# Kernel optimization log

Hardware: AMD Instinct MI355X
Metric: run time of the kernel (lower is better)

## Reference

```python
import jax, jax.numpy as jnp
import numpy as np

SQRT2 = 1.4142135623730951
T, B, C, H, W = 4, 8, 256, 32, 32
NB, D = 16, 16  # FL_blocks, block_size = dim // FL_blocks
VTH = 0.5       # all l1/l2 spike thresholds default to 0.5
TAUS = (0.01, 0.02, 0.02, 0.05)  # l2 channel-sparsity taus for LL,HL,LH,HH

# Heaviside spike with ATan surrogate gradient (spikingjelly default, alpha=2)
@jax.custom_vjp
def spike(x):
    return (x >= 0.0).astype(x.dtype)

def _spike_fwd(x):
    return spike(x), x

def _spike_bwd(x, g):
    alpha = 2.0
    sg = (alpha / 2.0) / (1.0 + (jnp.pi / 2.0 * alpha * x) ** 2)
    return (g * sg,)

spike.defvjp(_spike_fwd, _spike_bwd)

def lif(x, tau=2.0):
    # MultiStepLIFNode: v += (x - v)/tau, fire at vth=1, hard reset, detach_reset
    def step(v, xt):
        v = v + (xt - v) / tau
        s = spike(v - 1.0)
        v = v * (1.0 - jax.lax.stop_gradient(s))
        return v, s
    _, s = jax.lax.scan(step, jnp.zeros_like(x[0]), x)
    return s

def bn(x, g, b, eps=1e-5):
    # BatchNorm2d in training mode (batch statistics), x: (N,C,H,W)
    m = x.mean((0, 2, 3), keepdims=True)
    v = x.var((0, 2, 3), keepdims=True)
    return (x - m) / jnp.sqrt(v + eps) * g[None, :, None, None] + b[None, :, None, None]

def conv2d(x, w, b):
    y = jax.lax.conv_general_dilated(x, w, (1, 1), 'SAME',
                                     dimension_numbers=('NCHW', 'OIHW', 'NCHW'))
    return y + b[None, :, None, None]

def coeff_gate(c, vth):
    # spike-thresholded wavelet coefficient: keep coeff where |coeff| >= vth
    return c * spike(jnp.abs(c) - vth)

def channel_gate(c, tau):
    # 'channel' sparsity mode: drop whole channels whose mean energy < tau
    e = jnp.mean(c * c, axis=(0, 1, 3, 4))
    return c * spike(e - tau)[None, None, :, None, None]

def fwd(x, haar_weight, conv1_w, conv1_b, conv2_w, conv2_b,
        g_fwd, b_fwd, g_mul, b_mul, g_inv, b_inv, g_c1, b_c1, g_c2, b_c2):
    Tn, Bn, Cn, Hn, Wn = x.shape
    H2, W2 = Hn // 2, Wn // 2
    TB = Tn * Bn
    xs = lif(x)
    # level-1 Haar along W, spike-gated low/high subbands -> (T,B,2C,H,W/2)
    lo = (xs[..., 0::2] + xs[..., 1::2]) / SQRT2
    hi = (xs[..., 0::2] - xs[..., 1::2]) / SQRT2
    h1 = jnp.concatenate([coeff_gate(lo, VTH), coeff_gate(hi, VTH)], axis=2)
    h1 = bn(h1.reshape(TB, 2 * Cn, Hn, W2), g_fwd, b_fwd).reshape(Tn, Bn, 2 * Cn, Hn, W2)
    # level-2 Haar along H -> LL,HL,LH,HH each (T,B,C,H/2,W/2)
    L, Hc = h1[:, :, :Cn], h1[:, :, Cn:]
    def hh(t):
        return ((t[:, :, :, 0::2] + t[:, :, :, 1::2]) / SQRT2,
                (t[:, :, :, 0::2] - t[:, :, :, 1::2]) / SQRT2)
    LL, HL = hh(L)
    LH, HH = hh(Hc)
    subs = [channel_gate(coeff_gate(c, VTH), tau)
            for c, tau in zip((LL, HL, LH, HH), TAUS)]
    h2 = jnp.concatenate(subs, axis=2)  # (T,B,4C,H/2,W/2)
    h2 = bn(h2.reshape(TB, 4 * Cn, H2, W2), g_mul, b_mul).reshape(Tn, Bn, 4 * Cn, H2, W2)
    # block-diagonal mixing: exactly the torch reshape/permute/einsum path
    haar = h2.reshape(TB, NB, 4 * D, H2, W2).transpose(0, 3, 4, 1, 2)  # (TB,H2,W2,NB,4D)
    parts = [jnp.einsum('thwbd,bdk->thwbk', haar[..., i * D:(i + 1) * D], haar_weight)
             for i in range(4)]
    haar = jnp.concatenate(parts, axis=-1)
    haar = haar.reshape(TB, H2, W2, 4 * Cn).transpose(0, 3, 1, 2).reshape(Tn, Bn, 4 * Cn, H2, W2)
    # inverse 2-level Haar -> (T,B,C,H,W)
    LLr, HLr, LHr, HHr = (haar[:, :, i * Cn:(i + 1) * Cn] for i in range(4))
    def inv_h(a, b):
        e = (a + b) / SQRT2
        o = (a - b) / SQRT2
        return jnp.stack([e, o], axis=-2).reshape(Tn, Bn, Cn, Hn, W2)
    Lr = inv_h(LLr, HLr)
    Hr = inv_h(LHr, HHr)
    e = (Lr + Hr) / SQRT2
    o = (Lr - Hr) / SQRT2
    rec = jnp.stack([e, o], axis=-1).reshape(Tn, Bn, Cn, Hn, Wn)
    rec = bn(rec.reshape(TB, Cn, Hn, Wn), g_inv, b_inv).reshape(Tn, Bn, Cn, Hn, Wn)
    # per-block conv residual branches on the spike tensor
    xr = xs.reshape(TB * NB, D, Hn, Wn)
    c1 = bn(conv2d(xr, conv1_w, conv1_b).reshape(TB, Cn, Hn, Wn), g_c1, b_c1).reshape(Tn, Bn, Cn, Hn, Wn)
    c2 = bn(conv2d(xr, conv2_w, conv2_b).reshape(TB, Cn, Hn, Wn), g_c2, b_c2).reshape(Tn, Bn, Cn, Hn, Wn)
    return rec + c1 + c2

def setup_inputs() -> dict:
    key = jax.random.key(0)
    ks = jax.random.split(key, 4)
    return {
        'x': jax.random.normal(ks[0], (T, B, C, H, W), jnp.float32),
        'haar_weight': 0.02 * jax.random.normal(ks[1], (NB, D, D), jnp.float32),
        'conv1_w': 0.1 * jax.random.normal(ks[2], (D, D, 1, 1), jnp.float32),
        'conv1_b': jnp.zeros((D,), jnp.float32),
        'conv2_w': 0.05 * jax.random.normal(ks[3], (D, D, 3, 3), jnp.float32),
        'conv2_b': jnp.zeros((D,), jnp.float32),
        'g_fwd': jnp.ones((2 * C,), jnp.float32), 'b_fwd': jnp.zeros((2 * C,), jnp.float32),
        'g_mul': jnp.ones((4 * C,), jnp.float32), 'b_mul': jnp.zeros((4 * C,), jnp.float32),
        'g_inv': jnp.ones((C,), jnp.float32), 'b_inv': jnp.zeros((C,), jnp.float32),
        'g_c1': jnp.ones((C,), jnp.float32), 'b_c1': jnp.zeros((C,), jnp.float32),
        'g_c2': jnp.ones((C,), jnp.float32), 'b_c2': jnp.zeros((C,), jnp.float32),
    }

def reference(x, haar_weight, conv1_w, conv1_b, conv2_w, conv2_b,
              g_fwd, b_fwd, g_mul, b_mul, g_inv, b_inv, g_c1, b_c1, g_c2, b_c2):
    return fwd(x, haar_weight, conv1_w, conv1_b, conv2_w, conv2_b,
               g_fwd, b_fwd, g_mul, b_mul, g_inv, b_inv, g_c1, b_c1, g_c2, b_c2)
```

## Files before the change

kernel.cpp:

```cpp
#include <hip/hip_runtime.h>

#define T_ 4
#define B_ 8
#define C_ 256
#define TB_ 32
#define SQRT2_ 1.4142135623730951
#define INVS2_ 0.7071067811865475
#define EPS_ 1e-5

typedef __attribute__((ext_vector_type(8))) short short8;
typedef __attribute__((ext_vector_type(4))) float f32x4;

#define XST_OFF  ((size_t)0)
#define H1C_OFF  ((size_t)16777216)
#define COEF_OFF ((size_t)25165824)
#define ST_OFF   ((size_t)41943040)
#define WTAB_OFF ((size_t)42532864)
#define HIST_OFF ((size_t)42555392)
#define S3S 3072
#define S3Q 3328
#define S4S 3584
#define S4Q 3840
#define S5S 4096
#define S5Q 4352
#define NST 4608
#define NREP 16
#define NHREP 32

__device__ __forceinline__ unsigned short f2bf(float v) {
    union { float f; unsigned u; } x; x.f = v;
    unsigned r = x.u + 0x7FFFu + ((x.u >> 16) & 1u);
    return (unsigned short)(r >> 16);
}

__device__ __forceinline__ double st_sum(const double* __restrict__ st, int idx) {
    double s = 0.0;
    #pragma unroll
    for (int r = 0; r < NREP; ++r) s += st[r * NST + idx];
    return s;
}

__device__ __forceinline__ void mix_frags_q(const float* __restrict__ hw, int gbq, int lane, short8 am[4]) {
    const int o = lane & 15, g = lane >> 4;
    #pragma unroll
    for (int q = 0; q < 4; ++q) {
        #pragma unroll
        for (int e = 0; e < 8; ++e) {
            const int kk = g * 8 + e;
            unsigned short v = 0;
            if ((kk >> 4) == (q & 1)) {
                const int d = kk & 15;
                const int nbp = q * 4 + gbq;
                v = f2bf(hw[(nbp * 16 + d) * 16 + o]);
            }
            am[q][e] = (short)v;
        }
    }
}

__device__ __forceinline__ void conv_frags(const float* __restrict__ w1, const float* __restrict__ w2w,
                                           int lane, short8* awc2, short8& awc1) {
    const int o = lane & 15, g = lane >> 4, dA = (g & 1) * 8;
    #pragma unroll
    for (int m = 0; m < 5; ++m) {
        const int t = (m < 4) ? (2 * m + (g >> 1)) : 8;
        const bool act = (m < 4) || (g < 2);
        #pragma unroll
        for (int j = 0; j < 8; ++j) {
            const float wv = act ? w2w[(o * 16 + dA + j) * 9 + t] : 0.0f;
            awc2[m][j] = (short)f2bf(wv);
        }
    }
    #pragma unroll
    for (int j = 0; j < 8; ++j) {
        const float wv = (g < 2) ? w1[o * 16 + dA + j] : 0.0f;
        awc1[j] = (short)f2bf(wv);
    }
}

__device__ __forceinline__ void load_conv_frags(const unsigned short* __restrict__ convW,
                                                int lane, short8* awc2, short8& awc1) {
    #pragma unroll
    for (int m = 0; m < 5; ++m) awc2[m] = *(const short8*)&convW[(m * 64 + lane) * 8];
    awc1 = *(const short8*)&convW[(5 * 64 + lane) * 8];
}
__device__ __forceinline__ void load_mix_frags(const unsigned short* __restrict__ mixW,
                                               int gbq, int lane, short8 am[4]) {
    #pragma unroll
    for (int q = 0; q < 4; ++q) am[q] = *(const short8*)&mixW[((gbq * 4 + q) * 64 + lane) * 8];
}

__global__ __launch_bounds__(256) void k1_lif(const float* __restrict__ x,
                                              unsigned short* __restrict__ xsT,
                                              signed char* __restrict__ h1c,
                                              int* __restrict__ hist,
                                              double* __restrict__ st,
                                              const float* __restrict__ w1, const float* __restrict__ w2w,
                                              const float* __restrict__ hw,
                                              unsigned short* __restrict__ convW,
                                              unsigned short* __restrict__ mixW) {
    const int q = blockIdx.x & 3, nb = (blockIdx.x >> 2) & 15, b = blockIdx.x >> 6;
    const int tid = threadIdx.x;
    if (tid < 72) {
        double2 z2; z2.x = 0.0; z2.y = 0.0;
        *(double2*)(st + (size_t)blockIdx.x * 144 + tid * 2) = z2;
    }
    const int d = tid >> 4, pg = tid & 15;
    const int c = nb * 16 + d;
    const int h = q * 8 + (pg >> 1), wseg = (pg & 1) * 16;
    __shared__ __align__(16) char tr[8192];
    double v[16];
    #pragma unroll
    for (int i = 0; i < 16; ++i) v[i] = 0.0;
    unsigned long long cs = 0, cdd = 0, cu = 0, cv = 0;
    for (int t = 0; t < T_; ++t) {
        const size_t xi = ((size_t)((t * 8 + b) * 256 + c)) * 1024 + h * 32 + wseg;
        const float4* xp = (const float4*)(x + xi);
        int sp[16];
        #pragma unroll
        for (int q4 = 0; q4 < 4; ++q4) {
            const float4 xv = xp[q4];
            #pragma unroll
            for (int e = 0; e < 4; ++e) {
                const double xd = (e == 0 ? xv.x : e == 1 ? xv.y : e == 2 ? xv.z : xv.w);
                double vv = v[q4 * 4 + e];
                vv = vv + (xd - vv) * 0.5;
                const int s = (vv - 1.0 >= 0.0) ? 1 : 0;
                if (s) vv = 0.0;
                v[q4 * 4 + e] = vv;
                sp[q4 * 4 + e] = s;
            }
        }
        unsigned lo8[2] = {0u, 0u}, hi8[2] = {0u, 0u}, hp8[2] = {0u, 0u};
        #pragma unroll
        for (int pr = 0; pr < 8; ++pr) {
            const int lo = sp[2 * pr] + sp[2 * pr + 1];
            const int hi = sp[2 * pr] - sp[2 * pr + 1];
            const int sh = 8 * (pr & 3);
            lo8[pr >> 2] |= (unsigned)(lo & 0xFF) << sh;
            hi8[pr >> 2] |= (unsigned)(hi & 0xFF) << sh;
            hp8[pr >> 2] |= (unsigned)(hi + 1) << sh;
        }
        const size_t lob = ((size_t)((t * 8 + b) * 512 + c)) * 512 + h * 16 + (pg & 1) * 8;
        const size_t hib = ((size_t)((t * 8 + b) * 512 + 256 + c)) * 512 + h * 16 + (pg & 1) * 8;
        *(uint2*)(h1c + lob) = make_uint2(lo8[0], lo8[1]);
        *(uint2*)(h1c + hib) = make_uint2(hi8[0], hi8[1]);
        const unsigned plo0 = __shfl_xor(lo8[0], 2, 64);
        const unsigned plo1 = __shfl_xor(lo8[1], 2, 64);
        const unsigned php0 = __shfl_xor(hp8[0], 2, 64);
        const unsigned php1 = __shfl_xor(hp8[1], 2, 64);
        if (!(pg & 2)) {
            const unsigned sw0 = lo8[0] + plo0, sw1 = lo8[1] + plo1;
            const unsigned dw0 = lo8[0] + (0x02020202u - plo0), dw1 = lo8[1] + (0x02020202u - plo1);
            const unsigned uw0 = hp8[0] + php0, uw1 = hp8[1] + php1;
            const unsigned vw0 = hp8[0] + (0x02020202u - php0), vw1 = hp8[1] + (0x02020202u - php1);
            #pragma unroll
            for (int j = 0; j < 4; ++j) {
                const int sh = 8 * j;
                cs  += 1ull << (12 * ((sw0 >> sh) & 0x7));
                cs  += 1ull << (12 * ((sw1 >> sh) & 0x7));
                cdd += 1ull << (12 * ((dw0 >> sh) & 0x7));
                cdd += 1ull << (12 * ((dw1 >> sh) & 0x7));
                cu  += 1ull << (12 * ((uw0 >> sh) & 0x7));
                cu  += 1ull << (12 * ((uw1 >> sh) & 0x7));
                cv  += 1ull << (12 * ((vw0 >> sh) & 0x7));
                cv  += 1ull << (12 * ((vw1 >> sh) & 0x7));
            }
        }
        unsigned u[8];
        #pragma unroll
        for (int k = 0; k < 8; ++k)
            u[k] = (sp[2 * k] ? 0x3F80u : 0u) | (sp[2 * k + 1] ? 0x3F800000u : 0u);
        const int base = d * 512 + pg * 32;
        const int sw = (d & 3) << 4;
        *(uint4*)(tr + ((base) ^ sw))      = make_uint4(u[0], u[1], u[2], u[3]);
        *(uint4*)(tr + ((base + 16) ^ sw)) = make_uint4(u[4], u[5], u[6], u[7]);
        __syncthreads();
        {
            const int p = tid;
            unsigned o[8];
            #pragma unroll
            for (int dd = 0; dd < 8; ++dd) {
                const unsigned short a0 = *(const unsigned short*)(tr + (2 * dd) * 512 + (((p << 1)) ^ (((2 * dd) & 3) << 4)));
                const unsigned short a1 = *(const unsigned short*)(tr + (2 * dd + 1) * 512 + (((p << 1)) ^ (((2 * dd + 1) & 3) << 4)));
                o[dd] = (unsigned)a0 | ((unsigned)a1 << 16);
            }
            unsigned short* dst = xsT + (((size_t)((t * 8 + b) * 16 + nb)) * 1024 + q * 256 + p) * 16;
            *(uint4*)dst = make_uint4(o[0], o[1], o[2], o[3]);
            *(uint4*)(dst + 8) = make_uint4(o[4], o[5], o[6], o[7]);
        }
        __syncthreads();
    }
    #pragma unroll
    for (int m = 1; m < 16; m <<= 1) {
        {
            const unsigned a = __shfl_xor((unsigned)cs, m, 64);
            const unsigned bb2 = __shfl_xor((unsigned)(cs >> 32), m, 64);
            cs += ((unsigned long long)bb2 << 32) | a;
        }
        {
            const unsigned a = __shfl_xor((unsigned)cdd, m, 64);
            const unsigned bb2 = __shfl_xor((unsigned)(cdd >> 32), m, 64);
            cdd += ((unsigned long long)bb2 << 32) | a;
        }
        {
            const unsigned a = __shfl_xor((unsigned)cu, m, 64);
            const unsigned bb2 = __shfl_xor((unsigned)(cu >> 32), m, 64);
            cu += ((unsigned long long)bb2 << 32) | a;
        }
        {
            const unsigned a = __shfl_xor((unsigned)cv, m, 64);
            const unsigned bb2 = __shfl_xor((unsigned)(cv >> 32), m, 64);
            cv += ((unsigned long long)bb2 << 32) | a;
        }
    }
    if (pg == 0) {
        int* hh = hist + ((size_t)(b * 4 + q) * 20) * 256 + c;
        #pragma unroll
        for (int k = 0; k < 5; ++k) {
            hh[k * 256]         = (int)((cs  >> (12 * k)) & 0xFFF);
            hh[(5 + k) * 256]   = (int)((cdd >> (12 * k)) & 0xFFF);
            hh[(10 + k) * 256]  = (int)((cu  >> (12 * k)) & 0xFFF);
            hh[(15 + k) * 256]  = (int)((cv  >> (12 * k)) & 0xFFF);
        }
    }
    if (blockIdx.x == 0) {
        const int lane = tid & 63, grp = tid >> 6;
        if (grp == 0) {
            short8 awc2[5], awc1;
            conv_frags(w1, w2w, lane, awc2, awc1);
            #pragma unroll
            for (int m = 0; m < 5; ++m) *(short8*)&convW[(m * 64 + lane) * 8] = awc2[m];
            *(short8*)&convW[(5 * 64 + lane) * 8] = awc1;
        }
        short8 am[4];
        mix_frags_q(hw, grp, lane, am);
        #pragma unroll
        for (int qq = 0; qq < 4; ++qq) *(short8*)&mixW[((grp * 4 + qq) * 64 + lane) * 8] = am[qq];
    }
}

__device__ __forceinline__ void conv_tile(const unsigned short* tile, int lane, int h, int w0,
                                          const short8* awc2, const short8& awc1,
                                          f32x4& acc2o, f32x4& acc1o) {
    const int g = lane >> 4, n = lane & 15, dA = (g & 1) * 8;
    short8 bf[6];
    #pragma unroll
    for (int m = 0; m < 6; ++m) {
        const int t = (m < 4) ? (2 * m + (g >> 1)) : ((m == 4) ? 8 : 4);
        const int ky = t / 3, kx = t % 3;
        const int rr = h + ky, cc = w0 + n + kx;
        const int addr = (((rr * 34 + cc) * 32) + dA * 2) ^ ((cc & 4) << 2);
        bf[m] = *(const short8*)((const char*)tile + addr);
    }
    f32x4 acc2 = {0.f, 0.f, 0.f, 0.f};
    #pragma unroll
    for (int m = 0; m < 5; ++m)
        acc2 = __builtin_amdgcn_mfma_f32_16x16x32_bf16(awc2[m], bf[m], acc2, 0, 0, 0);
    const f32x4 z = {0.f, 0.f, 0.f, 0.f};
    acc1o = __builtin_amdgcn_mfma_f32_16x16x32_bf16(awc1, bf[5], z, 0, 0, 0);
    acc2o = acc2;
}

__device__ __forceinline__ void stage_rows(const unsigned short* __restrict__ src,
                                           int r0, int nr, int tid, unsigned short* tile) {
    const int total = nr * 34;
    for (int idx = tid; idx < total; idx += 256) {
        const int r = r0 + idx / 34, cpos = idx % 34;
        const int gh = r - 1, gw = cpos - 1;
        uint4 v0 = make_uint4(0u, 0u, 0u, 0u), v1 = v0;
        if (((unsigned)gh < 32u) & ((unsigned)gw < 32u)) {
            const char* sp = (const char*)(src + (size_t)(gh * 32 + gw) * 16);
            v0 = *(const uint4*)sp;
            v1 = *(const uint4*)(sp + 16);
        }
        const int base = ((r - r0) * 34 + cpos) * 32;
        const int sw = (cpos & 4) << 2;
        *(uint4*)((char*)tile + (base ^ sw)) = v0;
        *(uint4*)((char*)tile + ((base + 16) ^ sw)) = v1;
    }
}

__global__ __launch_bounds__(256) void kmid(const signed char* __restrict__ h1c,
                                            const unsigned short* __restrict__ xsT,
                                            double* __restrict__ st,
                                            char* __restrict__ coefD,
                                            const int* __restrict__ hist,
                                            const unsigned short* __restrict__ mixW,
                                            const unsigned short* __restrict__ convW,
                                            const float* __restrict__ g_fwd, const float* __restrict__ b_fwd,
                                            const float* __restrict__ g_mul, const float* __restrict__ b_mul) {
    __shared__ __align__(16) char smem[15232];
    const int tid = threadIdx.x, lane = tid & 63, wid = tid >> 6;
    if (blockIdx.x < 2048) {
        float* pad = (float*)smem;
        unsigned short* lutL = (unsigned short*)(smem + 512);
        int* histL = (int*)(smem + 1152);
        double* bn1L = (double*)(smem + 2432);
        signed char* rawL = (signed char*)(smem + 2944);
        unsigned short* coefL = (unsigned short*)(smem + 7040);
        const int pb = blockIdx.x & 3, gb = (blockIdx.x >> 2) & 15, tb = blockIdx.x >> 6;
        {
            const int ch = tid >> 3, o8 = (tid & 7) * 16;
            const int cab = (ch < 16) ? gb * 16 + ch : 256 + gb * 16 + (ch - 16);
            *(uint4*)(rawL + ch * 128 + o8) =
                *(const uint4*)(h1c + ((size_t)(tb * 512 + cab)) * 512 + pb * 128 + o8);
        }
        {
            const int i = tid & 15;
            const int c = gb * 16 + i;
            for (int kk = tid >> 4; kk < 20; kk += 16) {
                int s = 0;
                #pragma unroll
                for (int rep = 0; rep < NHREP; ++rep) s += hist[((size_t)(rep * 20 + kk)) * 256 + c];
                histL[i * 20 + kk] = s;
            }
        }
        __syncthreads();
        if (tid < 32) {
            const int i = tid & 15, hiF = tid >> 4;
            const int* hl = &histL[i * 20 + hiF * 10];
            double sc = 0.0, s2a = 0.0, s2b = 0.0;
            #pragma unroll
            for (int k = 0; k < 5; ++k) {
                const double c0 = (double)hl[k], c1 = (double)hl[5 + k];
                const int cval = hiF ? (k - 2) : k;
                sc += c0 * cval;
                s2a += c0 * (cval * cval);
                s2b += c1 * ((k - 2) * (k - 2));
            }
            const double sum = sc * INVS2_;
            const double sq = (0.5 * (s2a + s2b)) * 0.5;
            const double m = sum / 16384.0, var = sq / 16384.0 - m * m;
            const int gch = hiF * 256 + gb * 16 + i;
            const double a = (double)g_fwd[gch] / sqrt(var + EPS_);
            bn1L[hiF * 32 + i] = a * INVS2_;
            bn1L[hiF * 32 + 16 + i] = (double)b_fwd[gch] - m * a;
        }
        __syncthreads();
        if (tid < 64) {
            const int i = tid & 15, b4 = tid >> 4;
            const int hiF = b4 >> 1;
            const double A1 = bn1L[hiF * 32 + i], B1 = bn1L[hiF * 32 + 16 + i];
            const int* hl = &histL[i * 20 + b4 * 5];
            double gv[5], S = 0.0, Q = 0.0;
            #pragma unroll
            for (int k = 0; k < 5; ++k) {
                const int code = (b4 == 0) ? k : (k - 2);
                double val = ((b4 & 1) == 0) ? ((double)code * A1 + 2.0 * B1) * INVS2_
                                             : ((double)code * A1) * INVS2_;
                val = (fabs(val) - 0.5 >= 0.0) ? val : 0.0;
                gv[k] = val;
                const double cnt = (double)hl[k];
                S += cnt * val; Q += cnt * val * val;
            }
            const double e = Q / 8192.0;
            const double tau = (b4 == 0) ? 0.01 : (b4 == 3 ? 0.05 : 0.02);
            const int gch = b4 * 256 + gb * 16 + i;
            float A2, B2;
            if (e - tau >= 0.0) {
                const double m = S / 8192.0, var = Q / 8192.0 - m * m;
                const double a = (double)g_mul[gch] / sqrt(var + EPS_);
                A2 = (float)a; B2 = (float)((double)b_mul[gch] - m * a);
            } else { A2 = 0.0f; B2 = b_mul[gch]; }
            #pragma unroll
            for (int k = 0; k < 5; ++k)
                lutL[(i * 4 + b4) * 5 + k] = f2bf(fmaf((float)gv[k], A2, B2));
        }
        __syncthreads();
        {
            const int p = tid & 63, ds = tid >> 6;
            const int h2l = p >> 4, w2 = p & 15;
            unsigned pk[4][2];
            #pragma unroll
            for (int dd = 0; dd < 4; ++dd) {
                const int d = ds * 4 + dd;
                const int base = d * 128 + (2 * h2l) * 16 + w2;
                const int l0 = rawL[base], l1 = rawL[base + 16];
                const int q0 = rawL[2048 + base], q1 = rawL[2048 + base + 16];
                const unsigned short* lp = &lutL[d * 20];
                const unsigned hv[4] = { lp[l0 + l1],
                                         lp[5 + l0 - l1 + 2],
                                         lp[10 + q0 + q1 + 2],
                                         lp[15 + q0 - q1 + 2] };
                #pragma unroll
                for (int q = 0; q < 4; ++q) {
                    if (dd & 1) pk[q][dd >> 1] |= hv[q] << 16;
                    else        pk[q][dd >> 1] = hv[q];
                }
            }
            #pragma unroll
            for (int q = 0; q < 4; ++q) {
                const int slot = (((q & 1) * 2 + (ds >> 1)) ^ (p & 3));
                char* dst = (char*)coefL + (q >> 1) * 4096 + p * 64 + slot * 16 + (ds & 1) * 8;
                *(uint2*)dst = make_uint2(pk[q][0], pk[q][1]);
            }
        }
        short8 am[4];
        load_mix_frags(mixW, gb >> 2, lane, am);
        __syncthreads();
        {
            char* base = coefD + ((size_t)(tb * 16 + gb)) * 32768 + pb * 4096;
            const int i = tid * 32;
            const int pair = i >> 12, loc = i & 4095;
            *(uint4*)(base + pair * 16384 + loc) = *(const uint4*)((const char*)coefL + i);
            *(uint4*)(base + pair * 16384 + loc + 16) = *(const uint4*)((const char*)coefL + i + 16);
        }
        const int o = lane & 15, g = lane >> 4;
        const int Pl = wid * 16 + o;
        f32x4 Mh[4];
        #pragma unroll
        for (int p = 0; p < 2; ++p) {
            const int slot = g ^ (o & 3);
            const short8 bf = *(const short8*)((const char*)coefL + p * 4096 + Pl * 64 + slot * 16);
            const f32x4 z = {0.f, 0.f, 0.f, 0.f};
            Mh[2 * p]     = __builtin_amdgcn_mfma_f32_16x16x32_bf16(am[2 * p], bf, z, 0, 0, 0);
            Mh[2 * p + 1] = __builtin_amdgcn_mfma_f32_16x16x32_bf16(am[2 * p + 1], bf, z, 0, 0, 0);
        }
        float s2x[4], se[4];
        #pragma unroll
        for (int r = 0; r < 4; ++r) {
            s2x[r] = 2.0f * Mh[0][r];
            se[r] = Mh[0][r] * Mh[0][r] + Mh[1][r] * Mh[1][r] + Mh[2][r] * Mh[2][r] + Mh[3][r] * Mh[3][r];
        }
        #pragma unroll
        for (int r = 0; r < 4; ++r)
            #pragma unroll
            for (int m = 1; m < 16; m <<= 1) {
                s2x[r] += __shfl_xor(s2x[r], m, 64);
                se[r]  += __shfl_xor(se[r], m, 64);
            }
        if ((lane & 15) == 0) {
            #pragma unroll
            for (int r = 0; r < 4; ++r) {
                pad[(wid * 16 + g * 4 + r) * 2]     = s2x[r];
                pad[(wid * 16 + g * 4 + r) * 2 + 1] = se[r];
            }
        }
        __syncthreads();
        if (tid < 32) {
            const int j = tid >> 1, s = tid & 1;
            const float tot = pad[(0 * 16 + j) * 2 + s] + pad[(1 * 16 + j) * 2 + s]
                            + pad[(2 * 16 + j) * 2 + s] + pad[(3 * 16 + j) * 2 + s];
            double* stw = st + (((((tb & 3) << 2) | pb)) * NST);
            atomicAdd(&stw[(s ? S3Q : S3S) + gb * 16 + j], (double)tot);
        }
    } else {
        const int bid = blockIdx.x - 2048;
        const int hb = bid & 3, gb = (bid >> 2) & 15, tb = bid >> 6;
        unsigned short* tile = (unsigned short*)smem;
        float* pad = (float*)(smem + 10880);
        const unsigned short* src = xsT + (size_t)(tb * 16 + gb) * 1024 * 16;
        stage_rows(src, hb * 8, 10, tid, tile);
        short8 awc2[5], awc1;
        load_conv_frags(convW, lane, awc2, awc1);
        __syncthreads();
        float t1s[4] = {0, 0, 0, 0}, t1q[4] = {0, 0, 0, 0};
        float t2s[4] = {0, 0, 0, 0}, t2q[4] = {0, 0, 0, 0};
        #pragma unroll
        for (int ti = 0; ti < 4; ++ti) {
            const int lr = wid * 2 + (ti >> 1);
            const int w0 = (ti & 1) * 16;
            f32x4 a2v, a1v;
            conv_tile(tile, lane, lr, w0, awc2, awc1, a2v, a1v);
            #pragma unroll
            for (int r = 0; r < 4; ++r) {
                t1s[r] += a1v[r]; t1q[r] += a1v[r] * a1v[r];
                t2s[r] += a2v[r]; t2q[r] += a2v[r] * a2v[r];
            }
        }
        #pragma unroll
        for (int r = 0; r < 4; ++r)
            #pragma unroll
            for (int m = 1; m < 16; m <<= 1) {
                t1s[r] += __shfl_xor(t1s[r], m, 64);
                t1q[r] += __shfl_xor(t1q[r], m, 64);
                t2s[r] += __shfl_xor(t2s[r], m, 64);
                t2q[r] += __shfl_xor(t2q[r], m, 64);
            }
        if ((lane & 15) == 0) {
            const int G = lane >> 4;
            #pragma unroll
            for (int r = 0; r < 4; ++r) {
                const int oc = G * 4 + r;
                pad[(wid * 16 + oc) * 4 + 0] = t1s[r];
                pad[(wid * 16 + oc) * 4 + 1] = t1q[r];
                pad[(wid * 16 + oc) * 4 + 2] = t2s[r];
                pad[(wid * 16 + oc) * 4 + 3] = t2q[r];
            }
        }
        __syncthreads();
        if (tid < 64) {
            const int oc = tid >> 2, arr = tid & 3;
            const float vv = pad[(0 * 16 + oc) * 4 + arr] + pad[(1 * 16 + oc) * 4 + arr]
                           + pad[(2 * 16 + oc) * 4 + arr] + pad[(3 * 16 + oc) * 4 + arr];
            const int ch = gb * 16 + oc;
            const int off = (arr == 0 ? S4S : arr == 1 ? S4Q : arr == 2 ? S5S : S5Q) + ch;
            double* stw = st + (((((tb & 3) << 2) | hb)) * NST);
            atomicAdd(&stw[off], (double)vv);
        }
    }
}

__global__ __launch_bounds__(256) void kfin(const unsigned short* __restrict__ xsT,
                                            const char* __restrict__ coefD,
                                            const double* __restrict__ st,
                                            const unsigned short* __restrict__ convW,
                                            const unsigned short* __restrict__ mixW,
                                            const float* __restrict__ g_inv, const float* __restrict__ b_inv,
                                            const float* __restrict__ g_c1, const float* __restrict__ b_c1,
                                            const float* __restrict__ g_c2, const float* __restrict__ b_c2,
                                            const float* __restrict__ conv1_b, const float* __restrict__ conv2_b,
                                            float* __restrict__ out) {
    __shared__ __align__(16) char smem[36224];
    const int tid = threadIdx.x, lane = tid & 63, wid = tid >> 6;
    const int hf = blockIdx.x & 1, gb = (blockIdx.x >> 1) & 15, tb = blockIdx.x >> 5;
    unsigned short* tile  = (unsigned short*)smem;
    unsigned short* coefL = (unsigned short*)(smem + 19584);
    float* PA3 = (float*)(smem + 35968);
    float* PA4 = PA3 + 16; float* PA5 = PA3 + 32; float* PK = PA3 + 48;
    if (tid < 16) {
        const int oc = tid, c = gb * 16 + oc;
        const double n3 = 32768.0;
        const double s3 = st_sum(st, S3S + c), q3 = st_sum(st, S3Q + c);
        const double m3 = s3 / n3, var3 = q3 / n3 - m3 * m3;
        const double a3 = (double)g_inv[c] / sqrt(var3 + EPS_);
        const double bias1 = (double)conv1_b[oc];
        const double s4r = st_sum(st, S4S + c), q4r = st_sum(st, S4Q + c);
        const double s4 = s4r + n3 * bias1;
        const double q4v = q4r + 2.0 * bias1 * s4r + n3 * bias1 * bias1;
        const double m4 = s4 / n3, var4 = q4v / n3 - m4 * m4;
        const double a4 = (double)g_c1[c] / sqrt(var4 + EPS_);
        const double bias2 = (double)conv2_b[oc];
        const double s5r = st_sum(st, S5S + c), q5r = st_sum(st, S5Q + c);
        const double s5 = s5r + n3 * bias2;
        const double q5v = q5r + 2.0 * bias2 * s5r + n3 * bias2 * bias2;
        const double m5 = s5 / n3, var5 = q5v / n3 - m5 * m5;
        const double a5 = (double)g_c2[c] / sqrt(var5 + EPS_);
        PA3[oc] = (float)a3; PA4[oc] = (float)a4; PA5[oc] = (float)a5;
        PK[oc] = (float)(((double)b_inv[c] - m3 * a3) + ((double)b_c1[c] - m4 * a4)
                       + ((double)b_c2[c] - m5 * a5) + a4 * bias1 + a5 * bias2);
    }
    stage_rows(xsT + (size_t)(tb * 16 + gb) * 1024 * 16, hf * 16, 18, tid, tile);
    {
        const char* dump = coefD + ((size_t)(tb * 16 + gb)) * 32768 + hf * 8192;
        #pragma unroll
        for (int i = 0; i < 4; ++i)
            *(uint4*)((char*)coefL + i * 4096 + tid * 16) =
                *(const uint4*)(dump + (i >> 1) * 16384 + (i & 1) * 4096 + tid * 16);
    }
    short8 am[4], awc2[5], awc1;
    load_mix_frags(mixW, gb >> 2, lane, am);
    load_conv_frags(convW, lane, awc2, awc1);
    __syncthreads();
    const int G = lane >> 4, n = lane & 15;
    float fA3[4], fA4[4], fA5[4], fK[4];
    #pragma unroll
    for (int r = 0; r < 4; ++r) {
        const int oc = G * 4 + r;
        fA3[r] = PA3[oc]; fA4[r] = PA4[oc]; fA5[r] = PA5[oc]; fK[r] = PK[oc];
    }
    const float sw = (n & 1) ? -1.0f : 1.0f;
    #pragma unroll
    for (int hh2 = 0; hh2 < 2; ++hh2) {
        f32x4 Mh[4];
        {
            const int o = lane & 15, g = lane >> 4;
            const int Pl = (wid * 2 + hh2) * 16 + o;
            #pragma unroll
            for (int p = 0; p < 2; ++p) {
                const int slot = g ^ (o & 3);
                const short8 bf = *(const short8*)((const char*)coefL + p * 8192 + Pl * 64 + slot * 16);
                const f32x4 z = {0.f, 0.f, 0.f, 0.f};
                Mh[2 * p]     = __builtin_amdgcn_mfma_f32_16x16x32_bf16(am[2 * p], bf, z, 0, 0, 0);
                Mh[2 * p + 1] = __builtin_amdgcn_mfma_f32_16x16x32_bf16(am[2 * p + 1], bf, z, 0, 0, 0);
            }
        }
        #pragma unroll
        for (int w0h = 0; w0h < 2; ++w0h) {
            const int src = (lane & 48) + w0h * 8 + (n >> 1);
            float ms[4][4];
            #pragma unroll
            for (int q = 0; q < 4; ++q)
                #pragma unroll
                for (int r = 0; r < 4; ++r) ms[q][r] = __shfl(Mh[q][r], src, 64);
            #pragma unroll
            for (int hrow = 0; hrow < 2; ++hrow) {
                const float sh = hrow ? -1.0f : 1.0f;
                const int hl = wid * 4 + hh2 * 2 + hrow;
                const int hglob = hf * 16 + hl;
                const int w0 = w0h * 16;
                f32x4 a2v, a1v;
                conv_tile(tile, lane, hl, w0, awc2, awc1, a2v, a1v);
                #pragma unroll
                for (int r = 0; r < 4; ++r) {
                    const float rec = 0.5f * ((ms[0][r] + sh * ms[1][r]) + sw * (ms[2][r] + sh * ms[3][r]));
                    const int oc = G * 4 + r;
                    const size_t ai = ((size_t)(tb * 256 + gb * 16 + oc)) * 1024 + (size_t)hglob * 32 + w0 + n;
                    out[ai] = fA3[r] * rec + fA4[r] * a1v[r] + fA5[r] * a2v[r] + fK[r];
                }
            }
        }
    }
}

extern "C" void kernel_launch(void* const* d_in, const int* in_sizes, int n_in,
                              void* d_out, int out_size, void* d_ws, size_t ws_size,
                              hipStream_t stream) {
    const float* x        = (const float*)d_in[0];
    const float* haar_w   = (const float*)d_in[1];
    const float* conv1_w  = (const float*)d_in[2];
    const float* conv1_b  = (const float*)d_in[3];
    const float* conv2_w  = (const float*)d_in[4];
    const float* conv2_b  = (const float*)d_in[5];
    const float* g_fwd    = (const float*)d_in[6];
    const float* b_fwd    = (const float*)d_in[7];
    const float* g_mul    = (const float*)d_in[8];
    const float* b_mul    = (const float*)d_in[9];
    const float* g_inv    = (const float*)d_in[10];
    const float* b_inv    = (const float*)d_in[11];
    const float* g_c1     = (const float*)d_in[12];
    const float* b_c1     = (const float*)d_in[13];
    const float* g_c2     = (const float*)d_in[14];
    const float* b_c2     = (const float*)d_in[15];
    float* out = (float*)d_out;

    char* ws = (char*)d_ws;
    unsigned short* xsT = (unsigned short*)(ws + XST_OFF);
    signed char* h1c    = (signed char*)(ws + H1C_OFF);
    char* coefD         = ws + COEF_OFF;
    double* st          = (double*)(ws + ST_OFF);
    unsigned short* convW = (unsigned short*)(ws + WTAB_OFF);
    unsigned short* mixW  = (unsigned short*)(ws + WTAB_OFF + 6144);
    int* hist           = (int*)(ws + HIST_OFF);

    k1_lif<<<dim3(512), dim3(256), 0, stream>>>(x, xsT, h1c, hist, st,
                                                conv1_w, conv2_w, haar_w, convW, mixW);
    kmid<<<dim3(4096), dim3(256), 0, stream>>>(h1c, xsT, st, coefD, hist, mixW, convW,
                                               g_fwd, b_fwd, g_mul, b_mul);
    kfin<<<dim3(1024), dim3(256), 0, stream>>>(xsT, coefD, st, convW, mixW,
                                               g_inv, b_inv, g_c1, b_c1, g_c2, b_c2,
                                               conv1_b, conv2_b, out);
}
```

Before: 65.93 us.

## Recompute wavelet coefficients in kfin instead of round-tripping through global buffer

kmid no longer writes the bf16 subband coefficient tensor (coefD, 16 MB) to global memory. kfin instead reloads the compact int8 h1c codes, rebuilds the per-channel BN/gate lookup table through a shared lut_prologue helper, and regenerates the coefficients in shared memory. k1_lif also batches all four timesteps' transposes into a larger 32 KB shared buffer with a single barrier. This trades a large global write plus read for extra histogram reduction and LUT arithmetic in kfin, and the larger LDS footprint may lower k1 occupancy.

```diff
diff --git a/kernel.cpp b/kernel.cpp
--- a/kernel.cpp
+++ b/kernel.cpp
@@ -13,10 +13,9 @@
 
 #define XST_OFF  ((size_t)0)
 #define H1C_OFF  ((size_t)16777216)
-#define COEF_OFF ((size_t)25165824)
-#define ST_OFF   ((size_t)41943040)
-#define WTAB_OFF ((size_t)42532864)
-#define HIST_OFF ((size_t)42555392)
+#define ST_OFF   ((size_t)25165824)
+#define WTAB_OFF ((size_t)25755648)
+#define HIST_OFF ((size_t)25778176)
 #define S3S 3072
 #define S3Q 3328
 #define S4S 3584
@@ -108,11 +107,12 @@
     const int d = tid >> 4, pg = tid & 15;
     const int c = nb * 16 + d;
     const int h = q * 8 + (pg >> 1), wseg = (pg & 1) * 16;
-    __shared__ __align__(16) char tr[8192];
+    __shared__ __align__(16) char tr[32768];
     double v[16];
     #pragma unroll
     for (int i = 0; i < 16; ++i) v[i] = 0.0;
     unsigned long long cs = 0, cdd = 0, cu = 0, cv = 0;
+    #pragma unroll
     for (int t = 0; t < T_; ++t) {
         const size_t xi = ((size_t)((t * 8 + b) * 256 + c)) * 1024 + h * 32 + wseg;
         const float4* xp = (const float4*)(x + xi);
@@ -171,25 +171,26 @@
         #pragma unroll
         for (int k = 0; k < 8; ++k)
             u[k] = (sp[2 * k] ? 0x3F80u : 0u) | (sp[2 * k + 1] ? 0x3F800000u : 0u);
-        const int base = d * 512 + pg * 32;
+        const int base = t * 8192 + d * 512 + pg * 32;
         const int sw = (d & 3) << 4;
         *(uint4*)(tr + ((base) ^ sw))      = make_uint4(u[0], u[1], u[2], u[3]);
         *(uint4*)(tr + ((base + 16) ^ sw)) = make_uint4(u[4], u[5], u[6], u[7]);
-        __syncthreads();
-        {
-            const int p = tid;
-            unsigned o[8];
-            #pragma unroll
-            for (int dd = 0; dd < 8; ++dd) {
-                const unsigned short a0 = *(const unsigned short*)(tr + (2 * dd) * 512 + (((p << 1)) ^ (((2 * dd) & 3) << 4)));
-                const unsigned short a1 = *(const unsigned short*)(tr + (2 * dd + 1) * 512 + (((p << 1)) ^ (((2 * dd + 1) & 3) << 4)));
-                o[dd] = (unsigned)a0 | ((unsigned)a1 << 16);
-            }
-            unsigned short* dst = xsT + (((size_t)((t * 8 + b) * 16 + nb)) * 1024 + q * 256 + p) * 16;
-            *(uint4*)dst = make_uint4(o[0], o[1], o[2], o[3]);
-            *(uint4*)(dst + 8) = make_uint4(o[4], o[5], o[6], o[7]);
-        }
-        __syncthreads();
+    }
+    __syncthreads();
+    #pragma unroll
+    for (int t = 0; t < T_; ++t) {
+        const int p = tid;
+        unsigned o[8];
+        #pragma unroll
+        for (int dd = 0; dd < 8; ++dd) {
+            const char* sl = tr + t * 8192;
+            const unsigned short a0 = *(const unsigned short*)(sl + (2 * dd) * 512 + (((p << 1)) ^ (((2 * dd) & 3) << 4)));
+            const unsigned short a1 = *(const unsigned short*)(sl + (2 * dd + 1) * 512 + (((p << 1)) ^ (((2 * dd + 1) & 3) << 4)));
+            o[dd] = (unsigned)a0 | ((unsigned)a1 << 16);
+        }
+        unsigned short* dst = xsT + (((size_t)((t * 8 + b) * 16 + nb)) * 1024 + q * 256 + p) * 16;
+        *(uint4*)dst = make_uint4(o[0], o[1], o[2], o[3]);
+        *(uint4*)(dst + 8) = make_uint4(o[4], o[5], o[6], o[7]);
     }
     #pragma unroll
     for (int m = 1; m < 16; m <<= 1) {
@@ -238,6 +239,74 @@
         #pragma unroll
         for (int qq = 0; qq < 4; ++qq) *(short8*)&mixW[((grp * 4 + qq) * 64 + lane) * 8] = am[qq];
     }
+}
+
+__device__ __forceinline__ void lut_prologue(const int* __restrict__ hist, int gb, int tid,
+                                             const float* __restrict__ g_fwd, const float* __restrict__ b_fwd,
+                                             const float* __restrict__ g_mul, const float* __restrict__ b_mul,
+                                             int* histL, double* bn1L, unsigned short* lutL) {
+    {
+        const int i = tid & 15;
+        const int c = gb * 16 + i;
+        for (int kk = tid >> 4; kk < 20; kk += 16) {
+            int s = 0;
+            #pragma unroll
+            for (int rep = 0; rep < NHREP; ++rep) s += hist[((size_t)(rep * 20 + kk)) * 256 + c];
+            histL[i * 20 + kk] = s;
+        }
+    }
+    __syncthreads();
+    if (tid < 32) {
+        const int i = tid & 15, hiF = tid >> 4;
+        const int* hl = &histL[i * 20 + hiF * 10];
+        double sc = 0.0, s2a = 0.0, s2b = 0.0;
+        #pragma unroll
+        for (int k = 0; k < 5; ++k) {
+            const double c0 = (double)hl[k], c1 = (double)hl[5 + k];
+            const int cval = hiF ? (k - 2) : k;
+            sc += c0 * cval;
+            s2a += c0 * (cval * cval);
+            s2b += c1 * ((k - 2) * (k - 2));
+        }
+        const double sum = sc * INVS2_;
+        const double sq = (0.5 * (s2a + s2b)) * 0.5;
+        const double m = sum / 16384.0, var = sq / 16384.0 - m * m;
+        const int gch = hiF * 256 + gb * 16 + i;
+        const double a = (double)g_fwd[gch] / sqrt(var + EPS_);
+        bn1L[hiF * 32 + i] = a * INVS2_;
+        bn1L[hiF * 32 + 16 + i] = (double)b_fwd[gch] - m * a;
+    }
+    __syncthreads();
+    if (tid < 64) {
+        const int i = tid & 15, b4 = tid >> 4;
+        const int hiF = b4 >> 1;
+        const double A1 = bn1L[hiF * 32 + i], B1 = bn1L[hiF * 32 + 16 + i];
+        const int* hl = &histL[i * 20 + b4 * 5];
+        double gv[5], S = 0.0, Q = 0.0;
+        #pragma unroll
+        for (int k = 0; k < 5; ++k) {
+            const int code = (b4 == 0) ? k : (k - 2);
+            double val = ((b4 & 1) == 0) ? ((double)code * A1 + 2.0 * B1) * INVS2_
+                                         : ((double)code * A1) * INVS2_;
+            val = (fabs(val) - 0.5 >= 0.0) ? val : 0.0;
+            gv[k] = val;
+            const double cnt = (double)hl[k];
+            S += cnt * val; Q += cnt * val * val;
+        }
+        const double e = Q / 8192.0;
+        const double tau = (b4 == 0) ? 0.01 : (b4 == 3 ? 0.05 : 0.02);
+        const int gch = b4 * 256 + gb * 16 + i;
+        float A2, B2;
+        if (e - tau >= 0.0) {
+            const double m = S / 8192.0, var = Q / 8192.0 - m * m;
+            const double a = (double)g_mul[gch] / sqrt(var + EPS_);
+            A2 = (float)a; B2 = (float)((double)b_mul[gch] - m * a);
+        } else { A2 = 0.0f; B2 = b_mul[gch]; }
+        #pragma unroll
+        for (int k = 0; k < 5; ++k)
+            lutL[(i * 4 + b4) * 5 + k] = f2bf(fmaf((float)gv[k], A2, B2));
+    }
+    __syncthreads();
 }
 
 __device__ __forceinline__ void conv_tile(const unsigned short* tile, int lane, int h, int w0,
@@ -284,7 +353,6 @@
 __global__ __launch_bounds__(256) void kmid(const signed char* __restrict__ h1c,
                                             const unsigned short* __restrict__ xsT,
                                             double* __restrict__ st,
-                                            char* __restrict__ coefD,
                                             const int* __restrict__ hist,
                                             const unsigned short* __restrict__ mixW,
                                             const unsigned short* __restrict__ convW,
@@ -306,68 +374,7 @@
             *(uint4*)(rawL + ch * 128 + o8) =
                 *(const uint4*)(h1c + ((size_t)(tb * 512 + cab)) * 512 + pb * 128 + o8);
         }
-        {
-            const int i = tid & 15;
-            const int c = gb * 16 + i;
-            for (int kk = tid >> 4; kk < 20; kk += 16) {
-                int s = 0;
-                #pragma unroll
-                for (int rep = 0; rep < NHREP; ++rep) s += hist[((size_t)(rep * 20 + kk)) * 256 + c];
-                histL[i * 20 + kk] = s;
-            }
-        }
-        __syncthreads();
-        if (tid < 32) {
-            const int i = tid & 15, hiF = tid >> 4;
-            const int* hl = &histL[i * 20 + hiF * 10];
-            double sc = 0.0, s2a = 0.0, s2b = 0.0;
-            #pragma unroll
-            for (int k = 0; k < 5; ++k) {
-                const double c0 = (double)hl[k], c1 = (double)hl[5 + k];
-                const int cval = hiF ? (k - 2) : k;
-                sc += c0 * cval;
-                s2a += c0 * (cval * cval);
-                s2b += c1 * ((k - 2) * (k - 2));
-            }
-            const double sum = sc * INVS2_;
-            const double sq = (0.5 * (s2a + s2b)) * 0.5;
-            const double m = sum / 16384.0, var = sq / 16384.0 - m * m;
-            const int gch = hiF * 256 + gb * 16 + i;
-            const double a = (double)g_fwd[gch] / sqrt(var + EPS_);
-            bn1L[hiF * 32 + i] = a * INVS2_;
-            bn1L[hiF * 32 + 16 + i] = (double)b_fwd[gch] - m * a;
-        }
-        __syncthreads();
-        if (tid < 64) {
-            const int i = tid & 15, b4 = tid >> 4;
-            const int hiF = b4 >> 1;
-            const double A1 = bn1L[hiF * 32 + i], B1 = bn1L[hiF * 32 + 16 + i];
-            const int* hl = &histL[i * 20 + b4 * 5];
-            double gv[5], S = 0.0, Q = 0.0;
-            #pragma unroll
-            for (int k = 0; k < 5; ++k) {
-                const int code = (b4 == 0) ? k : (k - 2);
-                double val = ((b4 & 1) == 0) ? ((double)code * A1 + 2.0 * B1) * INVS2_
-                                             : ((double)code * A1) * INVS2_;
-                val = (fabs(val) - 0.5 >= 0.0) ? val : 0.0;
-                gv[k] = val;
-                const double cnt = (double)hl[k];
-                S += cnt * val; Q += cnt * val * val;
-            }
-            const double e = Q / 8192.0;
-            const double tau = (b4 == 0) ? 0.01 : (b4 == 3 ? 0.05 : 0.02);
-            const int gch = b4 * 256 + gb * 16 + i;
-            float A2, B2;
-            if (e - tau >= 0.0) {
-                const double m = S / 8192.0, var = Q / 8192.0 - m * m;
-                const double a = (double)g_mul[gch] / sqrt(var + EPS_);
-                A2 = (float)a; B2 = (float)((double)b_mul[gch] - m * a);
-            } else { A2 = 0.0f; B2 = b_mul[gch]; }
-            #pragma unroll
-            for (int k = 0; k < 5; ++k)
-                lutL[(i * 4 + b4) * 5 + k] = f2bf(fmaf((float)gv[k], A2, B2));
-        }
-        __syncthreads();
+        lut_prologue(hist, gb, tid, g_fwd, b_fwd, g_mul, b_mul, histL, bn1L, lutL);
         {
             const int p = tid & 63, ds = tid >> 6;
             const int h2l = p >> 4, w2 = p & 15;
@@ -399,13 +406,6 @@
         short8 am[4];
         load_mix_frags(mixW, gb >> 2, lane, am);
         __syncthreads();
-        {
-            char* base = coefD + ((size_t)(tb * 16 + gb)) * 32768 + pb * 4096;
-            const int i = tid * 32;
-            const int pair = i >> 12, loc = i & 4095;
-            *(uint4*)(base + pair * 16384 + loc) = *(const uint4*)((const char*)coefL + i);
-            *(uint4*)(base + pair * 16384 + loc + 16) = *(const uint4*)((const char*)coefL + i + 16);
-        }
         const int o = lane & 15, g = lane >> 4;
         const int Pl = wid * 16 + o;
         f32x4 Mh[4];
@@ -503,10 +503,13 @@
 }
 
 __global__ __launch_bounds__(256) void kfin(const unsigned short* __restrict__ xsT,
-                                            const char* __restrict__ coefD,
+                                            const signed char* __restrict__ h1c,
                                             const double* __restrict__ st,
+                                            const int* __restrict__ hist,
                                             const unsigned short* __restrict__ convW,
                                             const unsigned short* __restrict__ mixW,
+                                            const float* __restrict__ g_fwd, const float* __restrict__ b_fwd,
+                                            const float* __restrict__ g_mul, const float* __restrict__ b_mul,
                                             const float* __restrict__ g_inv, const float* __restrict__ b_inv,
                                             const float* __restrict__ g_c1, const float* __restrict__ b_c1,
                                             const float* __restrict__ g_c2, const float* __restrict__ b_c2,
@@ -515,8 +518,13 @@
     __shared__ __align__(16) char smem[36224];
     const int tid = threadIdx.x, lane = tid & 63, wid = tid >> 6;
     const int hf = blockIdx.x & 1, gb = (blockIdx.x >> 1) & 15, tb = blockIdx.x >> 5;
-    unsigned short* tile  = (unsigned short*)smem;
-    unsigned short* coefL = (unsigned short*)(smem + 19584);
+    unsigned short* coefL = (unsigned short*)smem;
+    char* regionA = smem + 16384;
+    signed char* rawL = (signed char*)regionA;
+    int* histL = (int*)(regionA + 8192);
+    double* bn1L = (double*)(regionA + 9472);
+    unsigned short* lutL = (unsigned short*)(regionA + 9984);
+    unsigned short* tile = (unsigned short*)regionA;
     float* PA3 = (float*)(smem + 35968);
     float* PA4 = PA3 + 16; float* PA5 = PA3 + 32; float* PK = PA3 + 48;
     if (tid < 16) {
@@ -541,14 +549,48 @@
         PK[oc] = (float)(((double)b_inv[c] - m3 * a3) + ((double)b_c1[c] - m4 * a4)
                        + ((double)b_c2[c] - m5 * a5) + a4 * bias1 + a5 * bias2);
     }
+    {
+        #pragma unroll
+        for (int it = 0; it < 2; ++it) {
+            const int idx = tid + it * 256;
+            const int ch = idx >> 4, off = (idx & 15) * 16;
+            const int cab = (ch < 16) ? gb * 16 + ch : 256 + gb * 16 + (ch - 16);
+            *(uint4*)(rawL + ch * 256 + off) =
+                *(const uint4*)(h1c + ((size_t)(tb * 512 + cab)) * 512 + hf * 256 + off);
+        }
+    }
+    lut_prologue(hist, gb, tid, g_fwd, b_fwd, g_mul, b_mul, histL, bn1L, lutL);
+    {
+        const int p = tid & 127, ds = tid >> 7;
+        const int h2l = p >> 4, w2 = p & 15;
+        unsigned pk[4][4];
+        #pragma unroll
+        for (int dd = 0; dd < 8; ++dd) {
+            const int d = ds * 8 + dd;
+            const int base = d * 256 + (2 * h2l) * 16 + w2;
+            const int l0 = rawL[base], l1 = rawL[base + 16];
+            const int q0 = rawL[4096 + base], q1 = rawL[4096 + base + 16];
+            const unsigned short* lp = &lutL[d * 20];
+            const unsigned hv[4] = { lp[l0 + l1],
+                                     lp[5 + l0 - l1 + 2],
+                                     lp[10 + q0 + q1 + 2],
+                                     lp[15 + q0 - q1 + 2] };
+            #pragma unroll
+            for (int q = 0; q < 4; ++q) {
+                if (dd & 1) pk[q][dd >> 1] |= hv[q] << 16;
+                else        pk[q][dd >> 1] = hv[q];
+            }
+        }
+        __syncthreads();
+        #pragma unroll
+        for (int q = 0; q < 4; ++q) {
+            const int slot = (((q & 1) * 2 + ds) ^ (p & 3));
+            char* dst = (char*)coefL + (q >> 1) * 8192 + p * 64 + slot * 16;
+            *(uint4*)dst = make_uint4(pk[q][0], pk[q][1], pk[q][2], pk[q][3]);
+        }
+    }
+    __syncthreads();
     stage_rows(xsT + (size_t)(tb * 16 + gb) * 1024 * 16, hf * 16, 18, tid, tile);
-    {
-        const char* dump = coefD + ((size_t)(tb * 16 + gb)) * 32768 + hf * 8192;
-        #pragma unroll
-        for (int i = 0; i < 4; ++i)
-            *(uint4*)((char*)coefL + i * 4096 + tid * 16) =
-                *(const uint4*)(dump + (i >> 1) * 16384 + (i & 1) * 4096 + tid * 16);
-    }
     short8 am[4], awc2[5], awc1;
     load_mix_frags(mixW, gb >> 2, lane, am);
     load_conv_frags(convW, lane, awc2, awc1);
@@ -628,7 +670,6 @@
     char* ws = (char*)d_ws;
     unsigned short* xsT = (unsigned short*)(ws + XST_OFF);
     signed char* h1c    = (signed char*)(ws + H1C_OFF);
-    char* coefD         = ws + COEF_OFF;
     double* st          = (double*)(ws + ST_OFF);
     unsigned short* convW = (unsigned short*)(ws + WTAB_OFF);
     unsigned short* mixW  = (unsigned short*)(ws + WTAB_OFF + 6144);
@@ -636,9 +677,10 @@
 
     k1_lif<<<dim3(512), dim3(256), 0, stream>>>(x, xsT, h1c, hist, st,
                                                 conv1_w, conv2_w, haar_w, convW, mixW);
-    kmid<<<dim3(4096), dim3(256), 0, stream>>>(h1c, xsT, st, coefD, hist, mixW, convW,
+    kmid<<<dim3(4096), dim3(256), 0, stream>>>(h1c, xsT, st, hist, mixW, convW,
                                                g_fwd, b_fwd, g_mul, b_mul);
-    kfin<<<dim3(1024), dim3(256), 0, stream>>>(xsT, coefD, st, convW, mixW,
+    kfin<<<dim3(1024), dim3(256), 0, stream>>>(xsT, h1c, st, hist, convW, mixW,
+                                               g_fwd, b_fwd, g_mul, b_mul,
                                                g_inv, b_inv, g_c1, b_c1, g_c2, b_c2,
                                                conv1_b, conv2_b, out);
 }
```

New measurement: 68.80 us. 4.4% more time.
